# Kernel optimization log

Measured on AMD Instinct MI355X. Metric: run time of the kernel, lower is better.

The kernel has to match this reference:

```python
import jax, jax.numpy as jnp
import numpy as np

N = 50000
NEG_SLOPE = 0.2


def gat_conv(x, src, dst, W, a_src, a_dst, bias, heads, out_ch, concat):
    n = x.shape[0]
    h = (x @ W).reshape(n, heads, out_ch)            # [N, H, C]
    alpha_s = jnp.einsum('nhc,hc->nh', h, a_src)      # [N, H]
    alpha_d = jnp.einsum('nhc,hc->nh', h, a_dst)
    e = alpha_s[src] + alpha_d[dst]                   # [E, H]
    e = jax.nn.leaky_relu(e, NEG_SLOPE)
    # segment softmax over destination node (PyG: softmax over index=dst)
    m = jax.ops.segment_max(e, dst, num_segments=n)
    e = jnp.exp(e - m[dst])
    s = jax.ops.segment_sum(e, dst, num_segments=n)
    alpha = e / (s[dst] + 1e-16)                      # [E, H]
    msg = h[src] * alpha[:, :, None]                  # [E, H, C]
    out = jax.ops.segment_sum(msg, dst, num_segments=n)  # [N, H, C]
    out = out.reshape(n, heads * out_ch) if concat else out.mean(axis=1)
    return out + bias


def setup_inputs() -> dict:
    key = jax.random.key(0)
    ks = jax.random.split(key, 12)
    F_in, H, C1, NC = 512, 8, 16, 64
    E = 800000
    x = jax.random.normal(ks[0], (N, F_in), dtype=jnp.float32)
    edge_index = jax.random.randint(ks[1], (2, E), 0, N, dtype=jnp.int64)
    def glorot(k, shape):
        fan = shape[0] + shape[-1]
        lim = jnp.sqrt(6.0 / fan).astype(jnp.float32)
        return jax.random.uniform(k, shape, jnp.float32, -lim, lim)
    W1 = glorot(ks[2], (F_in, H * C1))
    att_src1 = glorot(ks[3], (H, C1))
    att_dst1 = glorot(ks[4], (H, C1))
    b1 = jnp.zeros((H * C1,), jnp.float32)
    W2 = glorot(ks[5], (H * C1, NC))
    att_src2 = glorot(ks[6], (1, NC))
    att_dst2 = glorot(ks[7], (1, NC))
    b2 = jnp.zeros((NC,), jnp.float32)
    return {"x": x, "edge_index": edge_index,
            "W1": W1, "att_src1": att_src1, "att_dst1": att_dst1, "b1": b1,
            "W2": W2, "att_src2": att_src2, "att_dst2": att_dst2, "b2": b2}


def reference(x, edge_index, W1, att_src1, att_dst1, b1, W2, att_src2, att_dst2, b2):
    # PyG GATConv default add_self_loops=True
    loops = jnp.arange(N, dtype=edge_index.dtype)
    src = jnp.concatenate([edge_index[0], loops])
    dst = jnp.concatenate([edge_index[1], loops])
    h = gat_conv(x, src, dst, W1, att_src1, att_dst1, b1, heads=8, out_ch=16, concat=True)
    h = jax.nn.relu(h)
    out = gat_conv(h, src, dst, W2, att_src2, att_dst2, b2, heads=1, out_ch=64, concat=False)
    return jax.nn.log_softmax(out, axis=1)
```

## Files before the change

kernel.cpp:

```cpp
#include <hip/hip_runtime.h>
#include <math.h>

#define N_NODES 50000
#define FIN 512
#define H1 8
#define D1 128
#define D2 64
#define NSCB ((N_NODES + 1023) >> 10)
#define GG 1563

typedef __attribute__((ext_vector_type(4))) float f32x4;
typedef __attribute__((ext_vector_type(8))) __bf16 bf16x8;
typedef __attribute__((ext_vector_type(4))) __bf16 bf16x4;

__device__ __forceinline__ void gload_lds16(const void* g, void* l) {
    __builtin_amdgcn_global_load_lds(
        (const __attribute__((address_space(1))) void*)g,
        (__attribute__((address_space(3))) void*)l, 16, 0, 0);
}

__global__ __launch_bounds__(256) void k_prep(const float* __restrict__ W1,
                                              const float* __restrict__ W2,
                                              __bf16* __restrict__ WpP,
                                              __bf16* __restrict__ Wp2,
                                              int* __restrict__ cnt) {
    int idx = blockIdx.x * 256 + threadIdx.x;
    int k = idx >> 7, col = idx & 127;
    int region = k >> 6;
    int kgl = (k >> 3) & 7;
    int u_out = (kgl * 128 + col) ^ (kgl & 3);
    WpP[region * 8192 + u_out * 8 + (k & 7)] = (__bf16)W1[idx];
    if (idx < N_NODES) cnt[idx] = 0;
    if (idx < D1 * D2) {
        int k2 = idx >> 6, col2 = idx & 63;
        Wp2[(k2 >> 3) * 512 + col2 * 8 + (k2 & 7)] = (__bf16)W2[idx];
    }
}

__global__ __launch_bounds__(256) void k_mega(const float* __restrict__ x,
                                              const __bf16* __restrict__ WpP,
                                              const float* __restrict__ asrc1,
                                              const float* __restrict__ adst1,
                                              __bf16* __restrict__ h1b,
                                              float* __restrict__ as1,
                                              float* __restrict__ ad1,
                                              const int* __restrict__ ei, int E,
                                              int* __restrict__ cnt,
                                              int* __restrict__ rank) {
    __shared__ __align__(16) __bf16 As[2][32 * 64];
    __shared__ __align__(16) __bf16 Bs[2][64 * 128];
    const int t = threadIdx.x;

    if (blockIdx.x >= GG) {
        int e = (blockIdx.x - GG) * 256 + t;
        int ET = E + N_NODES;
        if (e < ET) {
            int d = (e < E) ? ei[E + e] : (e - E);
            rank[e] = atomicAdd(&cnt[d], 1);
        }
        return;
    }

    const int l = t & 63;
    const int w = t >> 6;
    const int wr = (w >> 1) * 16, wc = (w & 1) * 64;
    const int n0 = blockIdx.x * 32;

    f32x4 acc[4];
    #pragma unroll
    for (int j = 0; j < 4; ++j) acc[j] = (f32x4){0.f, 0.f, 0.f, 0.f};

    const int arow = t >> 4;
    const int ak4  = (t & 15) * 4;

    float4 fx[2];
    {
        const __bf16* gsrc = WpP;
        #pragma unroll
        for (int i = 0; i < 4; ++i) {
            int ubase = w * 256 + i * 64;
            gload_lds16(gsrc + (ubase + l) * 8, &Bs[0][ubase * 8]);
        }
        #pragma unroll
        for (int i = 0; i < 2; ++i) {
            int grow = n0 + arow + i * 16;
            fx[i] = (grow < N_NODES)
                ? *(const float4*)(x + (size_t)grow * FIN + ak4)
                : make_float4(0.f, 0.f, 0.f, 0.f);
        }
        #pragma unroll
        for (int i = 0; i < 2; ++i) {
            int row = arow + i * 16;
            bf16x4 v = {(__bf16)fx[i].x, (__bf16)fx[i].y,
                        (__bf16)fx[i].z, (__bf16)fx[i].w};
            int eo = (row * 64 + ak4) ^ ((row & 7) << 3);
            *(bf16x4*)(&As[0][0] + eo) = v;
        }
    }
    __syncthreads();

    for (int s = 0; s < 8; ++s) {
        const int cur = s & 1;
        float4 nfx[2];
        if (s < 7) {
            const int k0 = (s + 1) * 64;
            const __bf16* gsrc = WpP + (size_t)(s + 1) * 8192;
            #pragma unroll
            for (int i = 0; i < 4; ++i) {
                int ubase = w * 256 + i * 64;
                gload_lds16(gsrc + (ubase + l) * 8, &Bs[cur ^ 1][ubase * 8]);
            }
            #pragma unroll
            for (int i = 0; i < 2; ++i) {
                int grow = n0 + arow + i * 16;
                nfx[i] = (grow < N_NODES)
                    ? *(const float4*)(x + (size_t)grow * FIN + k0 + ak4)
                    : make_float4(0.f, 0.f, 0.f, 0.f);
            }
        }
        #pragma unroll
        for (int ks = 0; ks < 2; ++ks) {
            bf16x8 af, bfr[4];
            {
                int row = wr + (l & 15);
                int eo = (row * 64 + ks * 32 + (l >> 4) * 8) ^ ((row & 7) << 3);
                af = *(const bf16x8*)(&As[cur][0] + eo);
            }
            #pragma unroll
            for (int fn = 0; fn < 4; ++fn) {
                int col = wc + fn * 16 + (l & 15);
                int kg = ks * 4 + (l >> 4);
                int u = (kg * 128 + col) ^ (kg & 3);
                bfr[fn] = *(const bf16x8*)(&Bs[cur][0] + u * 8);
            }
            #pragma unroll
            for (int fn = 0; fn < 4; ++fn)
                acc[fn] = __builtin_amdgcn_mfma_f32_16x16x32_bf16(
                    af, bfr[fn], acc[fn], 0, 0, 0);
        }
        if (s < 7) {
            #pragma unroll
            for (int i = 0; i < 2; ++i) {
                int row = arow + i * 16;
                bf16x4 v = {(__bf16)nfx[i].x, (__bf16)nfx[i].y,
                            (__bf16)nfx[i].z, (__bf16)nfx[i].w};
                int eo = (row * 64 + ak4) ^ ((row & 7) << 3);
                *(bf16x4*)(&As[cur ^ 1][0] + eo) = v;
            }
        }
        __syncthreads();
    }
    #pragma unroll
    for (int reg = 0; reg < 4; ++reg) {
        int row = n0 + wr + (l >> 4) * 4 + reg;
        if (row >= N_NODES) continue;
        #pragma unroll
        for (int fn = 0; fn < 4; ++fn) {
            int col = wc + fn * 16 + (l & 15);
            h1b[(size_t)row * D1 + col] = (__bf16)acc[fn][reg];
        }
    }
    const int c16 = l & 15;
    float av[4], dv[4];
    #pragma unroll
    for (int fn = 0; fn < 4; ++fn) {
        int head = (wc >> 4) + fn;
        av[fn] = asrc1[head * 16 + c16];
        dv[fn] = adst1[head * 16 + c16];
    }
    #pragma unroll
    for (int reg = 0; reg < 4; ++reg) {
        #pragma unroll
        for (int fn = 0; fn < 4; ++fn) {
            float vs = acc[fn][reg] * av[fn];
            float vd = acc[fn][reg] * dv[fn];
            #pragma unroll
            for (int mk = 1; mk <= 8; mk <<= 1) {
                vs += __shfl_xor(vs, mk, 64);
                vd += __shfl_xor(vd, mk, 64);
            }
            if (c16 == 0) {
                int row = n0 + wr + (l >> 4) * 4 + reg;
                if (row < N_NODES) {
                    int head = (wc >> 4) + fn;
                    as1[(size_t)row * 8 + head] = vs;
                    ad1[(size_t)row * 8 + head] = vd;
                }
            }
        }
    }
}

__global__ __launch_bounds__(256) void k_scan1(const int* __restrict__ cnt,
                                               int* __restrict__ basep,
                                               int* __restrict__ aux) {
    __shared__ int lds[256];
    int t = threadIdx.x, b = blockIdx.x;
    int g = b * 1024 + t * 4;
    int v0 = (g + 0 < N_NODES) ? cnt[g + 0] : 0;
    int v1 = (g + 1 < N_NODES) ? cnt[g + 1] : 0;
    int v2 = (g + 2 < N_NODES) ? cnt[g + 2] : 0;
    int v3 = (g + 3 < N_NODES) ? cnt[g + 3] : 0;
    int tsum = v0 + v1 + v2 + v3;
    lds[t] = tsum; __syncthreads();
    for (int off = 1; off < 256; off <<= 1) {
        int add = (t >= off) ? lds[t - off] : 0;
        __syncthreads();
        lds[t] += add;
        __syncthreads();
    }
    int excl = lds[t] - tsum;
    if (g + 0 < N_NODES) basep[g + 0] = excl;
    if (g + 1 < N_NODES) basep[g + 1] = excl + v0;
    if (g + 2 < N_NODES) basep[g + 2] = excl + v0 + v1;
    if (g + 3 < N_NODES) basep[g + 3] = excl + v0 + v1 + v2;
    if (t == 255) aux[b] = lds[255];
}

__global__ __launch_bounds__(64) void k_scan2(const int* __restrict__ aux,
                                              int* __restrict__ auxs) {
    int t = threadIdx.x;
    int v = (t < NSCB) ? aux[t] : 0;
    int orig = v;
    for (int off = 1; off < 64; off <<= 1) {
        int x = __shfl_up(v, off, 64);
        if (t >= off) v += x;
    }
    auxs[t] = v - orig;
}

__global__ __launch_bounds__(256) void k_scan3(int* __restrict__ basep,
                                               const int* __restrict__ auxs, int ET) {
    int i = blockIdx.x * 256 + threadIdx.x;
    if (i < N_NODES) basep[i] += auxs[i >> 10];
    if (i == 0) basep[N_NODES] = ET;
}

__global__ __launch_bounds__(256) void k_scatter(const int* __restrict__ ei, int E,
                                                 const int* __restrict__ basep,
                                                 const int* __restrict__ rank,
                                                 int* __restrict__ srcs) {
    int e = blockIdx.x * 256 + threadIdx.x;
    int ET = E + N_NODES;
    if (e >= ET) return;
    int s = (e < E) ? ei[e] : (e - E);
    int d = (e < E) ? ei[E + e] : (e - E);
    srcs[basep[d] + rank[e]] = s;
}

__global__ __launch_bounds__(256) void k_agg1(const int* __restrict__ basep,
                                              const int* __restrict__ srcs,
                                              const float* __restrict__ as1,
                                              const float* __restrict__ ad1,
                                              const __bf16* __restrict__ h1b,
                                              const float* __restrict__ b1,
                                              __bf16* __restrict__ r1b) {
    __shared__ float elds[4][512];
    const int w = threadIdx.x >> 6;
    const int l = threadIdx.x & 63;
    const int q = l >> 4;
    const int c8 = (l & 15) * 8;
    const int h = (l & 15) >> 1;
    const int n = blockIdx.x * 4 + w;
    const int p0 = basep[n], p1 = basep[n + 1];
    const int m = p1 - p0;
    float adv[8];
    #pragma unroll
    for (int i = 0; i < 8; ++i) adv[i] = ad1[(size_t)n * 8 + i];
    float ac[8] = {0.f, 0.f, 0.f, 0.f, 0.f, 0.f, 0.f, 0.f};
    float se = 0.f;
    for (int base = 0; base < m; base += 64) {
        const int cm = min(64, m - base);
        asm volatile("s_waitcnt lgkmcnt(0)" ::: "memory");
        int my_s = 0;
        if (l < cm) {
            my_s = srcs[p0 + base + l];
            const float4* ap = (const float4*)(as1 + (size_t)my_s * 8);
            float4 A0 = ap[0], A1 = ap[1];
            float uu[8] = {A0.x + adv[0], A0.y + adv[1], A0.z + adv[2], A0.w + adv[3],
                           A1.x + adv[4], A1.y + adv[5], A1.z + adv[6], A1.w + adv[7]};
            float ee[8];
            #pragma unroll
            for (int i = 0; i < 8; ++i) {
                float u = uu[i];
                u = (u > 0.f) ? u : 0.2f * u;
                ee[i] = __expf(u);
            }
            *(float4*)(&elds[w][l * 8])     = make_float4(ee[0], ee[1], ee[2], ee[3]);
            *(float4*)(&elds[w][l * 8 + 4]) = make_float4(ee[4], ee[5], ee[6], ee[7]);
        }
        asm volatile("s_waitcnt lgkmcnt(0)" ::: "memory");
        #pragma unroll 2
        for (int j4 = 0; j4 < cm; j4 += 4) {
            int j = j4 + q;
            bool ok = j < cm;
            int jj = ok ? j : 0;
            int s = __shfl(my_s, jj, 64);
            float ee = elds[w][jj * 8 + h];
            if (!ok) ee = 0.f;
            se += ee;
            bf16x8 hv = *(const bf16x8*)(h1b + (size_t)s * D1 + c8);
            #pragma unroll
            for (int i = 0; i < 8; ++i) ac[i] += ee * (float)hv[i];
        }
    }
    #pragma unroll
    for (int mk = 16; mk <= 32; mk <<= 1) {
        #pragma unroll
        for (int i = 0; i < 8; ++i) ac[i] += __shfl_xor(ac[i], mk, 64);
        se += __shfl_xor(se, mk, 64);
    }
    if (q == 0) {
        float inv = 1.f / (se + 1e-16f);
        bf16x8 r;
        #pragma unroll
        for (int i = 0; i < 8; ++i)
            r[i] = (__bf16)fmaxf(ac[i] * inv + b1[c8 + i], 0.f);
        *(bf16x8*)(r1b + (size_t)n * D1 + c8) = r;
    }
}

__global__ __launch_bounds__(256) void k_gemm2(const __bf16* __restrict__ r1b,
                                               const __bf16* __restrict__ Wp2,
                                               const float* __restrict__ av2,
                                               const float* __restrict__ dv2,
                                               __bf16* __restrict__ h2b,
                                               float* __restrict__ as2,
                                               float* __restrict__ ad2) {
    __shared__ __align__(16) __bf16 As[128 * 128];
    __shared__ __align__(16) __bf16 Bs[128 * 64];
    const int t = threadIdx.x;
    const int l = t & 63;
    const int w = t >> 6;
    const int wr = w * 32;
    const int n0 = blockIdx.x * 128;

    const uint4* gb = (const uint4*)Wp2;
    #pragma unroll
    for (int i = 0; i < 4; ++i) {
        int u = t + i * 256;
        uint4 d = gb[u];
        int u2 = u ^ ((u >> 6) & 3);
        *(uint4*)(Bs + u2 * 8) = d;
    }
    #pragma unroll
    for (int i = 0; i < 8; ++i) {
        int u = t + i * 256;
        int row = u >> 4, koff = (u & 15) * 8;
        bf16x8 v = {};
        if (n0 + row < N_NODES)
            v = *(const bf16x8*)(r1b + (size_t)(n0 + row) * D1 + koff);
        int eo = (row * 128 + koff) ^ ((row & 7) << 3);
        *(bf16x8*)(As + eo) = v;
    }
    __syncthreads();

    f32x4 acc[2][4];
    #pragma unroll
    for (int i = 0; i < 2; ++i)
        #pragma unroll
        for (int j = 0; j < 4; ++j) acc[i][j] = (f32x4){0.f, 0.f, 0.f, 0.f};

    #pragma unroll
    for (int ks = 0; ks < 4; ++ks) {
        bf16x8 af[2], bfr[4];
        #pragma unroll
        for (int fm = 0; fm < 2; ++fm) {
            int row = wr + fm * 16 + (l & 15);
            int eo = (row * 128 + ks * 32 + (l >> 4) * 8) ^ ((row & 7) << 3);
            af[fm] = *(const bf16x8*)(As + eo);
        }
        #pragma unroll
        for (int fn = 0; fn < 4; ++fn) {
            int col = fn * 16 + (l & 15);
            int kg = ks * 4 + (l >> 4);
            int u = (kg * 64 + col) ^ (kg & 3);
            bfr[fn] = *(const bf16x8*)(Bs + u * 8);
        }
        #pragma unroll
        for (int fm = 0; fm < 2; ++fm)
            #pragma unroll
            for (int fn = 0; fn < 4; ++fn)
                acc[fm][fn] = __builtin_amdgcn_mfma_f32_16x16x32_bf16(
                    af[fm], bfr[fn], acc[fm][fn], 0, 0, 0);
    }
    #pragma unroll
    for (int fm = 0; fm < 2; ++fm) {
        #pragma unroll
        for (int reg = 0; reg < 4; ++reg) {
            int row = n0 + wr + fm * 16 + (l >> 4) * 4 + reg;
            if (row >= N_NODES) continue;
            #pragma unroll
            for (int fn = 0; fn < 4; ++fn) {
                int col = fn * 16 + (l & 15);
                h2b[(size_t)row * D2 + col] = (__bf16)acc[fm][fn][reg];
            }
        }
    }
    const int c16 = l & 15;
    float av[4], dv[4];
    #pragma unroll
    for (int fn = 0; fn < 4; ++fn) {
        av[fn] = av2[fn * 16 + c16];
        dv[fn] = dv2[fn * 16 + c16];
    }
    #pragma unroll
    for (int fm = 0; fm < 2; ++fm) {
        #pragma unroll
        for (int reg = 0; reg < 4; ++reg) {
            float vs = 0.f, vd = 0.f;
            #pragma unroll
            for (int fn = 0; fn < 4; ++fn) {
                vs += acc[fm][fn][reg] * av[fn];
                vd += acc[fm][fn][reg] * dv[fn];
            }
            #pragma unroll
            for (int mk = 1; mk <= 8; mk <<= 1) {
                vs += __shfl_xor(vs, mk, 64);
                vd += __shfl_xor(vd, mk, 64);
            }
            if (c16 == 0) {
                int row = n0 + wr + fm * 16 + (l >> 4) * 4 + reg;
                if (row < N_NODES) { as2[row] = vs; ad2[row] = vd; }
            }
        }
    }
}

__global__ __launch_bounds__(256) void k_agg2(const int* __restrict__ basep,
                                              const int* __restrict__ srcs,
                                              const float* __restrict__ as2,
                                              const float* __restrict__ ad2,
                                              const __bf16* __restrict__ h2b,
                                              const float* __restrict__ b2,
                                              float* __restrict__ out) {
    const int w = threadIdx.x >> 6;
    const int l = threadIdx.x & 63;
    const int o = l >> 3;
    const int c8 = (l & 7) * 8;
    const int n = blockIdx.x * 4 + w;
    const int p0 = basep[n], p1 = basep[n + 1];
    const int m = p1 - p0;
    const float adn = ad2[n];
    float ac[8] = {0.f, 0.f, 0.f, 0.f, 0.f, 0.f, 0.f, 0.f};
    float se = 0.f;
    for (int base = 0; base < m; base += 64) {
        const int cm = min(64, m - base);
        int my_s = 0; float my_e = 0.f;
        if (l < cm) {
            my_s = srcs[p0 + base + l];
            float u = as2[my_s] + adn;
            u = (u > 0.f) ? u : 0.2f * u;
            my_e = __expf(u);
        }
        #pragma unroll 2
        for (int j8 = 0; j8 < cm; j8 += 8) {
            int j = j8 + o;
            bool ok = j < cm;
            int jj = ok ? j : 0;
            int s = __shfl(my_s, jj, 64);
            float ee = __shfl(my_e, jj, 64);
            if (!ok) ee = 0.f;
            se += ee;
            bf16x8 hv = *(const bf16x8*)(h2b + (size_t)s * D2 + c8);
            #pragma unroll
            for (int i = 0; i < 8; ++i) ac[i] += ee * (float)hv[i];
        }
    }
    #pragma unroll
    for (int mk = 8; mk <= 32; mk <<= 1) {
        #pragma unroll
        for (int i = 0; i < 8; ++i) ac[i] += __shfl_xor(ac[i], mk, 64);
        se += __shfl_xor(se, mk, 64);
    }
    float inv = 1.f / (se + 1e-16f);
    float v[8];
    #pragma unroll
    for (int i = 0; i < 8; ++i) v[i] = ac[i] * inv + b2[c8 + i];
    float mx = v[0];
    #pragma unroll
    for (int i = 1; i < 8; ++i) mx = fmaxf(mx, v[i]);
    #pragma unroll
    for (int mk = 1; mk <= 4; mk <<= 1) mx = fmaxf(mx, __shfl_xor(mx, mk, 64));
    float ex = 0.f;
    #pragma unroll
    for (int i = 0; i < 8; ++i) ex += __expf(v[i] - mx);
    #pragma unroll
    for (int mk = 1; mk <= 4; mk <<= 1) ex += __shfl_xor(ex, mk, 64);
    float lse = mx + __logf(ex);
    if (o == 0) {
        f32x4 r0 = {v[0] - lse, v[1] - lse, v[2] - lse, v[3] - lse};
        f32x4 r1 = {v[4] - lse, v[5] - lse, v[6] - lse, v[7] - lse};
        *(f32x4*)(out + (size_t)n * D2 + c8)     = r0;
        *(f32x4*)(out + (size_t)n * D2 + c8 + 4) = r1;
    }
}

extern "C" void kernel_launch(void* const* d_in, const int* in_sizes, int n_in,
                              void* d_out, int out_size, void* d_ws, size_t ws_size,
                              hipStream_t stream) {
    const float* x     = (const float*)d_in[0];
    const int*   ei    = (const int*)d_in[1];
    const float* W1    = (const float*)d_in[2];
    const float* asrc1 = (const float*)d_in[3];
    const float* adst1 = (const float*)d_in[4];
    const float* b1    = (const float*)d_in[5];
    const float* W2    = (const float*)d_in[6];
    const float* asrc2 = (const float*)d_in[7];
    const float* adst2 = (const float*)d_in[8];
    const float* b2    = (const float*)d_in[9];

    const int E  = in_sizes[1] / 2;
    const int ET = E + N_NODES;

    __bf16* r1b = (__bf16*)d_ws;
    float* fw  = (float*)(r1b + (size_t)N_NODES * D1);
    float* as1  = fw;
    float* ad1  = as1  + (size_t)N_NODES * H1;
    float* as2  = ad1  + (size_t)N_NODES * H1;
    float* ad2  = as2  + N_NODES;
    int* iw   = (int*)(ad2 + N_NODES);
    int* cnt  = iw;
    int* basep= cnt  + N_NODES;
    int* aux  = basep + N_NODES + 1;
    int* auxs = aux  + 64;
    int* rank = auxs + 64;
    int* srcs = rank + ET;
    uintptr_t pa = ((uintptr_t)(srcs + ET) + 255) & ~(uintptr_t)255;
    __bf16* WpP  = (__bf16*)pa;
    __bf16* Wp2  = WpP + (size_t)FIN * D1;
    __bf16* h1b  = Wp2 + (size_t)D1 * D2;
    __bf16* h2b  = h1b + (size_t)N_NODES * D1;

    const int gE = (ET + 255) / 256;
    const int gN = (N_NODES + 255) / 256;

    k_prep   <<<FIN * D1 / 256, 256, 0, stream>>>(W1, W2, WpP, Wp2, cnt);
    k_mega   <<<GG + gE, 256, 0, stream>>>(x, WpP, asrc1, adst1, h1b, as1, ad1,
                                           ei, E, cnt, rank);
    k_scan1  <<<NSCB, 256, 0, stream>>>(cnt, basep, aux);
    k_scan2  <<<1, 64, 0, stream>>>(aux, auxs);
    k_scan3  <<<gN, 256, 0, stream>>>(basep, auxs, ET);
    k_scatter<<<gE, 256, 0, stream>>>(ei, E, basep, rank, srcs);

    k_agg1   <<<N_NODES / 4, 256, 0, stream>>>(basep, srcs, as1, ad1, h1b, b1, r1b);
    k_gemm2  <<<(N_NODES + 127) / 128, 256, 0, stream>>>(r1b, Wp2, asrc2, adst2, h2b, as2, ad2);
    k_agg2   <<<N_NODES / 4, 256, 0, stream>>>(basep, srcs, as2, ad2, h2b, b2, (float*)d_out);
}
```

Measured before the change: 159.8 us.

## Single-buffer GEMM1 LDS tiles and fold scan fixup into consumers

The first-layer GEMM drops its double-buffered LDS and register prefetch in favour of a simple load-sync-compute loop. This halves LDS use, which could raise occupancy, but it gives up overlap of global loads with MFMA work. The k_scan3 launch is removed: the scatter and both aggregation kernels now add the block offset from auxs themselves and use ET for the last node's end. The scatter also writes srcs with nontemporal stores.

```diff
diff --git a/kernel.cpp b/kernel.cpp
--- a/kernel.cpp
+++ b/kernel.cpp
@@ -47,8 +47,8 @@
                                               const int* __restrict__ ei, int E,
                                               int* __restrict__ cnt,
                                               int* __restrict__ rank) {
-    __shared__ __align__(16) __bf16 As[2][32 * 64];
-    __shared__ __align__(16) __bf16 Bs[2][64 * 128];
+    __shared__ __align__(16) __bf16 As[32 * 64];
+    __shared__ __align__(16) __bf16 Bs[64 * 128];
     const int t = threadIdx.x;
 
     if (blockIdx.x >= GG) {
@@ -73,80 +73,47 @@
     const int arow = t >> 4;
     const int ak4  = (t & 15) * 4;
 
-    float4 fx[2];
-    {
-        const __bf16* gsrc = WpP;
-        #pragma unroll
-        for (int i = 0; i < 4; ++i) {
-            int ubase = w * 256 + i * 64;
-            gload_lds16(gsrc + (ubase + l) * 8, &Bs[0][ubase * 8]);
-        }
-        #pragma unroll
-        for (int i = 0; i < 2; ++i) {
-            int grow = n0 + arow + i * 16;
-            fx[i] = (grow < N_NODES)
-                ? *(const float4*)(x + (size_t)grow * FIN + ak4)
-                : make_float4(0.f, 0.f, 0.f, 0.f);
+    for (int s = 0; s < 8; ++s) {
+        const int k0 = s * 64;
+        {
+            const __bf16* gsrc = WpP + (size_t)s * 8192;
+            #pragma unroll
+            for (int i = 0; i < 4; ++i) {
+                int ubase = w * 256 + i * 64;
+                gload_lds16(gsrc + (ubase + l) * 8, Bs + ubase * 8);
+            }
         }
         #pragma unroll
         for (int i = 0; i < 2; ++i) {
             int row = arow + i * 16;
-            bf16x4 v = {(__bf16)fx[i].x, (__bf16)fx[i].y,
-                        (__bf16)fx[i].z, (__bf16)fx[i].w};
+            int grow = n0 + row;
+            float4 f = {0.f, 0.f, 0.f, 0.f};
+            if (grow < N_NODES)
+                f = *(const float4*)(x + (size_t)grow * FIN + k0 + ak4);
+            bf16x4 v = {(__bf16)f.x, (__bf16)f.y, (__bf16)f.z, (__bf16)f.w};
             int eo = (row * 64 + ak4) ^ ((row & 7) << 3);
-            *(bf16x4*)(&As[0][0] + eo) = v;
-        }
-    }
-    __syncthreads();
-
-    for (int s = 0; s < 8; ++s) {
-        const int cur = s & 1;
-        float4 nfx[2];
-        if (s < 7) {
-            const int k0 = (s + 1) * 64;
-            const __bf16* gsrc = WpP + (size_t)(s + 1) * 8192;
-            #pragma unroll
-            for (int i = 0; i < 4; ++i) {
-                int ubase = w * 256 + i * 64;
-                gload_lds16(gsrc + (ubase + l) * 8, &Bs[cur ^ 1][ubase * 8]);
-            }
-            #pragma unroll
-            for (int i = 0; i < 2; ++i) {
-                int grow = n0 + arow + i * 16;
-                nfx[i] = (grow < N_NODES)
-                    ? *(const float4*)(x + (size_t)grow * FIN + k0 + ak4)
-                    : make_float4(0.f, 0.f, 0.f, 0.f);
-            }
-        }
+            *(bf16x4*)(As + eo) = v;
+        }
+        __syncthreads();
         #pragma unroll
         for (int ks = 0; ks < 2; ++ks) {
             bf16x8 af, bfr[4];
             {
                 int row = wr + (l & 15);
                 int eo = (row * 64 + ks * 32 + (l >> 4) * 8) ^ ((row & 7) << 3);
-                af = *(const bf16x8*)(&As[cur][0] + eo);
+                af = *(const bf16x8*)(As + eo);
             }
             #pragma unroll
             for (int fn = 0; fn < 4; ++fn) {
                 int col = wc + fn * 16 + (l & 15);
                 int kg = ks * 4 + (l >> 4);
                 int u = (kg * 128 + col) ^ (kg & 3);
-                bfr[fn] = *(const bf16x8*)(&Bs[cur][0] + u * 8);
+                bfr[fn] = *(const bf16x8*)(Bs + u * 8);
             }
             #pragma unroll
             for (int fn = 0; fn < 4; ++fn)
                 acc[fn] = __builtin_amdgcn_mfma_f32_16x16x32_bf16(
                     af, bfr[fn], acc[fn], 0, 0, 0);
-        }
-        if (s < 7) {
-            #pragma unroll
-            for (int i = 0; i < 2; ++i) {
-                int row = arow + i * 16;
-                bf16x4 v = {(__bf16)nfx[i].x, (__bf16)nfx[i].y,
-                            (__bf16)nfx[i].z, (__bf16)nfx[i].w};
-                int eo = (row * 64 + ak4) ^ ((row & 7) << 3);
-                *(bf16x4*)(&As[cur ^ 1][0] + eo) = v;
-            }
         }
         __syncthreads();
     }
@@ -229,15 +196,9 @@
     auxs[t] = v - orig;
 }
 
-__global__ __launch_bounds__(256) void k_scan3(int* __restrict__ basep,
-                                               const int* __restrict__ auxs, int ET) {
-    int i = blockIdx.x * 256 + threadIdx.x;
-    if (i < N_NODES) basep[i] += auxs[i >> 10];
-    if (i == 0) basep[N_NODES] = ET;
-}
-
 __global__ __launch_bounds__(256) void k_scatter(const int* __restrict__ ei, int E,
                                                  const int* __restrict__ basep,
+                                                 const int* __restrict__ auxs,
                                                  const int* __restrict__ rank,
                                                  int* __restrict__ srcs) {
     int e = blockIdx.x * 256 + threadIdx.x;
@@ -245,16 +206,18 @@
     if (e >= ET) return;
     int s = (e < E) ? ei[e] : (e - E);
     int d = (e < E) ? ei[E + e] : (e - E);
-    srcs[basep[d] + rank[e]] = s;
+    int pos = basep[d] + auxs[d >> 10] + rank[e];
+    __builtin_nontemporal_store(s, &srcs[pos]);
 }
 
 __global__ __launch_bounds__(256) void k_agg1(const int* __restrict__ basep,
+                                              const int* __restrict__ auxs,
                                               const int* __restrict__ srcs,
                                               const float* __restrict__ as1,
                                               const float* __restrict__ ad1,
                                               const __bf16* __restrict__ h1b,
                                               const float* __restrict__ b1,
-                                              __bf16* __restrict__ r1b) {
+                                              __bf16* __restrict__ r1b, int ET) {
     __shared__ float elds[4][512];
     const int w = threadIdx.x >> 6;
     const int l = threadIdx.x & 63;
@@ -262,7 +225,8 @@
     const int c8 = (l & 15) * 8;
     const int h = (l & 15) >> 1;
     const int n = blockIdx.x * 4 + w;
-    const int p0 = basep[n], p1 = basep[n + 1];
+    const int p0 = basep[n] + auxs[n >> 10];
+    const int p1 = (n + 1 < N_NODES) ? basep[n + 1] + auxs[(n + 1) >> 10] : ET;
     const int m = p1 - p0;
     float adv[8];
     #pragma unroll
@@ -428,18 +392,20 @@
 }
 
 __global__ __launch_bounds__(256) void k_agg2(const int* __restrict__ basep,
+                                              const int* __restrict__ auxs,
                                               const int* __restrict__ srcs,
                                               const float* __restrict__ as2,
                                               const float* __restrict__ ad2,
                                               const __bf16* __restrict__ h2b,
                                               const float* __restrict__ b2,
-                                              float* __restrict__ out) {
+                                              float* __restrict__ out, int ET) {
     const int w = threadIdx.x >> 6;
     const int l = threadIdx.x & 63;
     const int o = l >> 3;
     const int c8 = (l & 7) * 8;
     const int n = blockIdx.x * 4 + w;
-    const int p0 = basep[n], p1 = basep[n + 1];
+    const int p0 = basep[n] + auxs[n >> 10];
+    const int p1 = (n + 1 < N_NODES) ? basep[n + 1] + auxs[(n + 1) >> 10] : ET;
     const int m = p1 - p0;
     const float adn = ad2[n];
     float ac[8] = {0.f, 0.f, 0.f, 0.f, 0.f, 0.f, 0.f, 0.f};
@@ -533,17 +499,15 @@
     __bf16* h2b  = h1b + (size_t)N_NODES * D1;
 
     const int gE = (ET + 255) / 256;
-    const int gN = (N_NODES + 255) / 256;
 
     k_prep   <<<FIN * D1 / 256, 256, 0, stream>>>(W1, W2, WpP, Wp2, cnt);
     k_mega   <<<GG + gE, 256, 0, stream>>>(x, WpP, asrc1, adst1, h1b, as1, ad1,
                                            ei, E, cnt, rank);
     k_scan1  <<<NSCB, 256, 0, stream>>>(cnt, basep, aux);
     k_scan2  <<<1, 64, 0, stream>>>(aux, auxs);
-    k_scan3  <<<gN, 256, 0, stream>>>(basep, auxs, ET);
-    k_scatter<<<gE, 256, 0, stream>>>(ei, E, basep, rank, srcs);
-
-    k_agg1   <<<N_NODES / 4, 256, 0, stream>>>(basep, srcs, as1, ad1, h1b, b1, r1b);
+    k_scatter<<<gE, 256, 0, stream>>>(ei, E, basep, auxs, rank, srcs);
+
+    k_agg1   <<<N_NODES / 4, 256, 0, stream>>>(basep, auxs, srcs, as1, ad1, h1b, b1, r1b, ET);
     k_gemm2  <<<(N_NODES + 127) / 128, 256, 0, stream>>>(r1b, Wp2, asrc2, adst2, h2b, as2, ad2);
-    k_agg2   <<<N_NODES / 4, 256, 0, stream>>>(basep, srcs, as2, ad2, h2b, b2, (float*)d_out);
-}
+    k_agg2   <<<N_NODES / 4, 256, 0, stream>>>(basep, auxs, srcs, as2, ad2, h2b, b2, (float*)d_out, ET);
+}
```

Measured after the change: 161.2 us. No clear change (+0.9%).
